# Performance work log

Hardware: AMD Instinct MI355X
Metric: run time of the kernel (lower is better)

Reference implementation:

```python
import jax, jax.numpy as jnp
import numpy as np

B, P, D, H, U, C = 32, 196, 512, 8, 4, 500

def setup_inputs() -> dict:
    key = jax.random.key(0)
    ks = jax.random.split(key, 12)
    s = 0.02
    return {
        "patch_embeddings": jax.random.normal(ks[0], (B, P, D), jnp.float32),
        "global_features": jax.random.normal(ks[1], (B, D), jnp.float32),
        "query_vectors": jax.random.normal(ks[2], (H, D), jnp.float32) * s,
        "dom_W": jax.random.normal(ks[3], (D, D), jnp.float32) / np.sqrt(D),
        "dom_b": jnp.zeros((D,), jnp.float32),
        "sem_W": jax.random.normal(ks[4], (H, D, D), jnp.float32) / np.sqrt(D),
        "sem_b": jnp.zeros((H, D), jnp.float32),
        "unknown_semantic_tokens": jax.random.normal(ks[5], (U, D), jnp.float32) * s,
        "known_prefix": jax.random.normal(ks[6], (C, 1, D), jnp.float32) * s,   # SOS embedding per class
        "known_suffix": jax.random.normal(ks[7], (C, 1, D), jnp.float32) * s,   # last-token embedding per class
        "unk_prefix": jax.random.normal(ks[8], (1, D), jnp.float32) * s,
        "unk_suffix": jax.random.normal(ks[9], (1, D), jnp.float32) * s,
    }


def reference(patch_embeddings, global_features, query_vectors, dom_W, dom_b,
              sem_W, sem_b, unknown_semantic_tokens, known_prefix, known_suffix,
              unk_prefix, unk_suffix):
    b, p, d = patch_embeddings.shape
    h = query_vectors.shape[0]
    c = known_prefix.shape[0]
    u = unknown_semantic_tokens.shape[0]

    # SemanticTokenExtractor: per-head attention over patches (vectorized over heads)
    scores = jnp.einsum('bpd,hd->bph', patch_embeddings, query_vectors)      # [B,P,H]
    weights = jax.nn.softmax(scores, axis=1)                                  # softmax over patches
    semantic_tokens = jnp.einsum('bph,bpd->bhd', weights, patch_embeddings)   # [B,H,D]

    # DomainTokenGenerator (2D input -> identity) + domain projection (torch Linear: x @ W.T + b)
    projected_domain = global_features @ dom_W.T + dom_b                      # [B,D]

    # Per-head semantic projections: head k uses its own Linear
    projected_sem = jnp.einsum('bhd,hed->bhe', semantic_tokens, sem_W) + sem_b  # [B,H,D]

    # Known prompts: for each (b, c): [prefix_c(1), domain_b(1), semantics_b(H), suffix_c(1)]
    pre = jnp.broadcast_to(known_prefix[None], (b, c, 1, d))
    dom = jnp.broadcast_to(projected_domain[:, None, None, :], (b, c, 1, d))
    sem = jnp.broadcast_to(projected_sem[:, None], (b, c, h, d))
    suf = jnp.broadcast_to(known_suffix[None], (b, c, 1, d))
    known_prompts = jnp.concatenate([pre, dom, sem, suf], axis=2).reshape(b * c, h + 3, d)

    # Unknown prompts: [unk_prefix(1), domain_b(1), unknown_semantic_tokens(U), unk_suffix(1)]
    upre = jnp.broadcast_to(unk_prefix[None], (b, 1, d))
    udom = projected_domain[:, None, :]
    usem = jnp.broadcast_to(unknown_semantic_tokens[None], (b, u, d))
    usuf = jnp.broadcast_to(unk_suffix[None], (b, 1, d))
    unknown_prompts = jnp.concatenate([upre, udom, usem, usuf], axis=1)       # [B, U+3, D]

    return known_prompts, unknown_prompts, semantic_tokens
```

## Files before the change

kernel.cpp:

```cpp
#include <hip/hip_runtime.h>

typedef unsigned int uint32;
typedef uint32 v4u __attribute__((ext_vector_type(4)));

#define Bb 32
#define Pp 196
#define Dd 512
#define Hh 8
#define Uu 4
#define Cc 500

#define OUT1_ELEM_OFF 90112000
#define OUT2_ELEM_OFF 90226688

#define NPC 16

#define WS_SC   0
#define WS_PART 51200
#define WS_DOM  2148352
#define WS_SEM  2164736

__device__ __forceinline__ float dot4(float4 a, float4 b, float acc) {
    acc = fmaf(a.x, b.x, acc);
    acc = fmaf(a.y, b.y, acc);
    acc = fmaf(a.z, b.z, acc);
    acc = fmaf(a.w, b.w, acc);
    return acc;
}

__global__ __launch_bounds__(256)
void k_scores(const float* __restrict__ patch, const float* __restrict__ query,
              float* __restrict__ sc) {
    __shared__ float s_q[Hh * Dd];
    const int b = blockIdx.x / 49;
    const int p0 = (blockIdx.x % 49) * 4;
    const int tid = threadIdx.x;
    for (int j = tid; j < Hh * Dd / 4; j += 256)
        ((float4*)s_q)[j] = ((const float4*)query)[j];
    __syncthreads();

    const int wave = tid >> 6, lane = tid & 63;
    const int p = p0 + wave;
    const float* pr = patch + ((size_t)b * Pp + p) * Dd + lane * 8;
    const float4 v0 = *(const float4*)pr;
    const float4 v1 = *(const float4*)(pr + 4);

    float out = 0.f;
#pragma unroll
    for (int h = 0; h < 8; ++h) {
        const float4 q0 = *(const float4*)&s_q[h * Dd + lane * 8];
        const float4 q1 = *(const float4*)&s_q[h * Dd + lane * 8 + 4];
        float a = dot4(v0, q0, 0.f);
        a = dot4(v1, q1, a);
#pragma unroll
        for (int m = 32; m >= 1; m >>= 1) a += __shfl_xor(a, m, 64);
        if (lane == h) out = a;
    }
    if (lane < 8) sc[((size_t)b * Hh + lane) * Pp + p] = out;
}

__global__ __launch_bounds__(256)
void k_pool_part(const float* __restrict__ patch, const float* __restrict__ sc,
                 float* __restrict__ part) {
    __shared__ float s_w[Hh * Pp];
    const int b = blockIdx.x >> 4;
    const int pc = blockIdx.x & 15;
    const int tid = threadIdx.x;

    for (int j = tid; j < Hh * Pp; j += 256) s_w[j] = sc[(size_t)b * Hh * Pp + j];
    __syncthreads();

    {
        const int h = tid >> 5, gl = tid & 31;
        float m = -1e30f;
        for (int p = gl; p < Pp; p += 32) m = fmaxf(m, s_w[h * Pp + p]);
#pragma unroll
        for (int mm = 16; mm >= 1; mm >>= 1) m = fmaxf(m, __shfl_xor(m, mm, 64));
        float s = 0.f;
        for (int p = gl; p < Pp; p += 32) s += __expf(s_w[h * Pp + p] - m);
#pragma unroll
        for (int mm = 16; mm >= 1; mm >>= 1) s += __shfl_xor(s, mm, 64);
        const float inv = 1.f / s;
        for (int p = gl; p < Pp; p += 32)
            s_w[h * Pp + p] = __expf(s_w[h * Pp + p] - m) * inv;
    }
    __syncthreads();

    const int f = tid & 127;
    const int hq = tid >> 7;
    const int pstart = pc * 13;
    const int pend = (pstart + 13 < Pp) ? pstart + 13 : Pp;
    float4 a0 = {0, 0, 0, 0}, a1 = a0, a2 = a0, a3 = a0;
    const float4* pb4 = (const float4*)(patch + (size_t)b * Pp * Dd);
    for (int p = pstart; p < pend; ++p) {
        const float4 pv = pb4[p * 128 + f];
        const float w0 = s_w[(hq * 4 + 0) * Pp + p];
        const float w1 = s_w[(hq * 4 + 1) * Pp + p];
        const float w2 = s_w[(hq * 4 + 2) * Pp + p];
        const float w3 = s_w[(hq * 4 + 3) * Pp + p];
        a0.x = fmaf(w0, pv.x, a0.x); a0.y = fmaf(w0, pv.y, a0.y);
        a0.z = fmaf(w0, pv.z, a0.z); a0.w = fmaf(w0, pv.w, a0.w);
        a1.x = fmaf(w1, pv.x, a1.x); a1.y = fmaf(w1, pv.y, a1.y);
        a1.z = fmaf(w1, pv.z, a1.z); a1.w = fmaf(w1, pv.w, a1.w);
        a2.x = fmaf(w2, pv.x, a2.x); a2.y = fmaf(w2, pv.y, a2.y);
        a2.z = fmaf(w2, pv.z, a2.z); a2.w = fmaf(w2, pv.w, a2.w);
        a3.x = fmaf(w3, pv.x, a3.x); a3.y = fmaf(w3, pv.y, a3.y);
        a3.z = fmaf(w3, pv.z, a3.z); a3.w = fmaf(w3, pv.w, a3.w);
    }
    float4* po = (float4*)part + ((size_t)b * NPC + pc) * 1024;
    po[(hq * 4 + 0) * 128 + f] = a0;
    po[(hq * 4 + 1) * 128 + f] = a1;
    po[(hq * 4 + 2) * 128 + f] = a2;
    po[(hq * 4 + 3) * 128 + f] = a3;
}

__global__ __launch_bounds__(256)
void k_combine(const float* __restrict__ part, float* __restrict__ st) {
    const int idx = blockIdx.x * 256 + threadIdx.x;
    const int b = idx >> 10;
    const int r = idx & 1023;
    const float4* p4 = (const float4*)part;
    float4 a = {0, 0, 0, 0};
#pragma unroll
    for (int pc = 0; pc < NPC; ++pc) {
        const float4 v = p4[((size_t)b * NPC + pc) * 1024 + r];
        a.x += v.x; a.y += v.y; a.z += v.z; a.w += v.w;
    }
    ((float4*)st)[idx] = a;
}

#define PJS 513
__global__ __launch_bounds__(256)
void k_proj(const float* __restrict__ gf, const float* __restrict__ domW,
            const float* __restrict__ domb, const float* __restrict__ semW,
            const float* __restrict__ semb, const float* __restrict__ st,
            float* __restrict__ dom_ws, float* __restrict__ sem_ws) {
    __shared__ float s_w[32 * PJS];
    __shared__ float s_st[32 * PJS];
    const int blk = blockIdx.x;
    const int tid = threadIdx.x;
    if (blk < 128) {
        const int h = blk >> 4;
        const int e0 = (blk & 15) * 32;
        for (int g = tid; g < 32 * 128; g += 256) {
            const int r = g >> 7, c4 = g & 127;
            const float4 w = ((const float4*)semW)[((size_t)(h * Dd + e0 + r)) * 128 + c4];
            float* dw = &s_w[r * PJS + c4 * 4];
            dw[0] = w.x; dw[1] = w.y; dw[2] = w.z; dw[3] = w.w;
            const float4 s = ((const float4*)st)[((size_t)(r * Hh + h)) * 128 + c4];
            float* ds = &s_st[r * PJS + c4 * 4];
            ds[0] = s.x; ds[1] = s.y; ds[2] = s.z; ds[3] = s.w;
        }
        __syncthreads();
        const int pe = tid & 15;
        const int pb = tid >> 4;
        const float* w0r = &s_w[(2 * pe) * PJS];
        const float* w1r = &s_w[(2 * pe + 1) * PJS];
        const float* s0r = &s_st[(2 * pb) * PJS];
        const float* s1r = &s_st[(2 * pb + 1) * PJS];
        float a00 = 0.f, a01 = 0.f, a10 = 0.f, a11 = 0.f;
#pragma unroll 8
        for (int d = 0; d < Dd; ++d) {
            const float w0 = w0r[d], w1 = w1r[d];
            const float s0 = s0r[d], s1 = s1r[d];
            a00 = fmaf(s0, w0, a00);
            a01 = fmaf(s0, w1, a01);
            a10 = fmaf(s1, w0, a10);
            a11 = fmaf(s1, w1, a11);
        }
        const int e_ = e0 + 2 * pe;
        const float b0 = semb[h * Dd + e_], b1 = semb[h * Dd + e_ + 1];
        float* o0 = &sem_ws[((2 * pb) * Hh + h) * Dd + e_];
        float* o1 = &sem_ws[((2 * pb + 1) * Hh + h) * Dd + e_];
        o0[0] = a00 + b0; o0[1] = a01 + b1;
        o1[0] = a10 + b0; o1[1] = a11 + b1;
    } else {
        const int tg = (blk - 128) * 256 + tid;
        const int b = tg >> 9;
        const int e = tg & 511;
        const float4* wr = (const float4*)(domW + (size_t)e * Dd);
        const float4* gr = (const float4*)(gf + (size_t)b * Dd);
        float acc = domb[e];
#pragma unroll 8
        for (int j = 0; j < Dd / 4; ++j) acc = dot4(gr[j], wr[j], acc);
        dom_ws[b * Dd + e] = acc;
    }
}

__global__ __launch_bounds__(256)
void k_assemble(const v4u* __restrict__ pre, const v4u* __restrict__ suf,
                const v4u* __restrict__ dom, const v4u* __restrict__ sem,
                const v4u* __restrict__ upre, const v4u* __restrict__ usuf,
                const v4u* __restrict__ ust,
                v4u* __restrict__ out0, v4u* __restrict__ out1) {
    const int blk = blockIdx.x;
    const int tid = threadIdx.x;
    if (blk < 16000) {
        const int b = blk / 500;
        const int c = blk % 500;
        v4u* row = out0 + (size_t)blk * 1408;
#pragma unroll
        for (int k = 0; k < 6; ++k) {
            const int i = tid + k * 256;
            if (k < 5 || i < 1408) {
                const int t = i >> 7;
                const int off = i & 127;
                v4u v;
                if (t == 0) v = pre[c * 128 + off];
                else if (t == 10) v = suf[c * 128 + off];
                else if (t == 1) v = dom[b * 128 + off];
                else v = sem[b * 1024 + (t - 2) * 128 + off];
                row[i] = v;
            }
        }
    } else {
        const int b = blk - 16000;
#pragma unroll
        for (int k = 0; k < 4; ++k) {
            const int i = tid + k * 256;
            if (k < 3 || i < 896) {
                const int t = i >> 7;
                const int off = i & 127;
                v4u v;
                if (t == 0) v = upre[off];
                else if (t == 6) v = usuf[off];
                else if (t == 1) v = dom[b * 128 + off];
                else v = ust[(t - 2) * 128 + off];
                out1[b * 896 + i] = v;
            }
        }
    }
}

extern "C" void kernel_launch(void* const* d_in, const int* in_sizes, int n_in,
                              void* d_out, int out_size, void* d_ws, size_t ws_size,
                              hipStream_t stream) {
    const float* patch = (const float*)d_in[0];
    const float* gf    = (const float*)d_in[1];
    const float* query = (const float*)d_in[2];
    const float* domW  = (const float*)d_in[3];
    const float* domb  = (const float*)d_in[4];
    const float* semW  = (const float*)d_in[5];
    const float* semb  = (const float*)d_in[6];
    const float* ust   = (const float*)d_in[7];
    const float* pre   = (const float*)d_in[8];
    const float* suf   = (const float*)d_in[9];
    const float* upre  = (const float*)d_in[10];
    const float* usuf  = (const float*)d_in[11];

    float* out = (float*)d_out;
    float* st_out = out + OUT2_ELEM_OFF;

    float* ws   = (float*)d_ws;
    float* sc_w = ws + WS_SC;
    float* part = ws + WS_PART;
    float* domp = ws + WS_DOM;
    float* semp = ws + WS_SEM;

    hipLaunchKernelGGL(k_scores, dim3(Bb * 49), dim3(256), 0, stream, patch, query, sc_w);
    hipLaunchKernelGGL(k_pool_part, dim3(Bb * NPC), dim3(256), 0, stream, patch, sc_w, part);
    hipLaunchKernelGGL(k_combine, dim3(128), dim3(256), 0, stream, part, st_out);
    hipLaunchKernelGGL(k_proj, dim3(192), dim3(256), 0, stream,
                       gf, domW, domb, semW, semb, st_out, domp, semp);
    hipLaunchKernelGGL(k_assemble, dim3(16032), dim3(256), 0, stream,
                       (const v4u*)pre, (const v4u*)suf,
                       (const v4u*)domp, (const v4u*)semp,
                       (const v4u*)upre, (const v4u*)usuf, (const v4u*)ust,
                       (v4u*)out, (v4u*)(out + OUT1_ELEM_OFF));
}
```

Baseline: 434.6 us.

## Restructure pooling, split-K semantic projection, and reorder assemble block mapping

Pooling blocks now use 128 threads, each accumulating all 8 heads, so every patch row is read once per block instead of twice. The semantic projection splits the reduction dimension in two across more blocks, using float4 shared tiles and a 4x2 register tile, and adds a small kernel that sums the partials and applies the bias. The assemble kernel moves to 128-thread blocks with one token row per iteration, and interleaves classes across consecutive blocks so the same batch's domain and semantic rows are reused. The cost is an extra kernel launch and a partial-sum buffer in workspace. Assemble, a write-bound copy of about 360 MB, dominates the run time.

```diff
diff --git a/kernel.cpp b/kernel.cpp
--- a/kernel.cpp
+++ b/kernel.cpp
@@ -19,6 +19,7 @@
 #define WS_PART 51200
 #define WS_DOM  2148352
 #define WS_SEM  2164736
+#define WS_PP   2295808
 
 __device__ __forceinline__ float dot4(float4 a, float4 b, float acc) {
     acc = fmaf(a.x, b.x, acc);
@@ -59,7 +60,7 @@
     if (lane < 8) sc[((size_t)b * Hh + lane) * Pp + p] = out;
 }
 
-__global__ __launch_bounds__(256)
+__global__ __launch_bounds__(128)
 void k_pool_part(const float* __restrict__ patch, const float* __restrict__ sc,
                  float* __restrict__ part) {
     __shared__ float s_w[Hh * Pp];
@@ -67,51 +68,46 @@
     const int pc = blockIdx.x & 15;
     const int tid = threadIdx.x;
 
-    for (int j = tid; j < Hh * Pp; j += 256) s_w[j] = sc[(size_t)b * Hh * Pp + j];
+    for (int j = tid; j < Hh * Pp; j += 128) s_w[j] = sc[(size_t)b * Hh * Pp + j];
     __syncthreads();
 
     {
-        const int h = tid >> 5, gl = tid & 31;
+        const int h = tid >> 4, gl = tid & 15;
         float m = -1e30f;
-        for (int p = gl; p < Pp; p += 32) m = fmaxf(m, s_w[h * Pp + p]);
-#pragma unroll
-        for (int mm = 16; mm >= 1; mm >>= 1) m = fmaxf(m, __shfl_xor(m, mm, 64));
+        for (int p = gl; p < Pp; p += 16) m = fmaxf(m, s_w[h * Pp + p]);
+#pragma unroll
+        for (int mm = 8; mm >= 1; mm >>= 1) m = fmaxf(m, __shfl_xor(m, mm, 64));
         float s = 0.f;
-        for (int p = gl; p < Pp; p += 32) s += __expf(s_w[h * Pp + p] - m);
-#pragma unroll
-        for (int mm = 16; mm >= 1; mm >>= 1) s += __shfl_xor(s, mm, 64);
+        for (int p = gl; p < Pp; p += 16) s += __expf(s_w[h * Pp + p] - m);
+#pragma unroll
+        for (int mm = 8; mm >= 1; mm >>= 1) s += __shfl_xor(s, mm, 64);
         const float inv = 1.f / s;
-        for (int p = gl; p < Pp; p += 32)
+        for (int p = gl; p < Pp; p += 16)
             s_w[h * Pp + p] = __expf(s_w[h * Pp + p] - m) * inv;
     }
     __syncthreads();
 
-    const int f = tid & 127;
-    const int hq = tid >> 7;
+    const int f = tid;
     const int pstart = pc * 13;
     const int pend = (pstart + 13 < Pp) ? pstart + 13 : Pp;
-    float4 a0 = {0, 0, 0, 0}, a1 = a0, a2 = a0, a3 = a0;
+    float4 acc[8];
+#pragma unroll
+    for (int h = 0; h < 8; ++h) acc[h] = (float4){0, 0, 0, 0};
     const float4* pb4 = (const float4*)(patch + (size_t)b * Pp * Dd);
     for (int p = pstart; p < pend; ++p) {
         const float4 pv = pb4[p * 128 + f];
-        const float w0 = s_w[(hq * 4 + 0) * Pp + p];
-        const float w1 = s_w[(hq * 4 + 1) * Pp + p];
-        const float w2 = s_w[(hq * 4 + 2) * Pp + p];
-        const float w3 = s_w[(hq * 4 + 3) * Pp + p];
-        a0.x = fmaf(w0, pv.x, a0.x); a0.y = fmaf(w0, pv.y, a0.y);
-        a0.z = fmaf(w0, pv.z, a0.z); a0.w = fmaf(w0, pv.w, a0.w);
-        a1.x = fmaf(w1, pv.x, a1.x); a1.y = fmaf(w1, pv.y, a1.y);
-        a1.z = fmaf(w1, pv.z, a1.z); a1.w = fmaf(w1, pv.w, a1.w);
-        a2.x = fmaf(w2, pv.x, a2.x); a2.y = fmaf(w2, pv.y, a2.y);
-        a2.z = fmaf(w2, pv.z, a2.z); a2.w = fmaf(w2, pv.w, a2.w);
-        a3.x = fmaf(w3, pv.x, a3.x); a3.y = fmaf(w3, pv.y, a3.y);
-        a3.z = fmaf(w3, pv.z, a3.z); a3.w = fmaf(w3, pv.w, a3.w);
+#pragma unroll
+        for (int h = 0; h < 8; ++h) {
+            const float w = s_w[h * Pp + p];
+            acc[h].x = fmaf(w, pv.x, acc[h].x);
+            acc[h].y = fmaf(w, pv.y, acc[h].y);
+            acc[h].z = fmaf(w, pv.z, acc[h].z);
+            acc[h].w = fmaf(w, pv.w, acc[h].w);
+        }
     }
     float4* po = (float4*)part + ((size_t)b * NPC + pc) * 1024;
-    po[(hq * 4 + 0) * 128 + f] = a0;
-    po[(hq * 4 + 1) * 128 + f] = a1;
-    po[(hq * 4 + 2) * 128 + f] = a2;
-    po[(hq * 4 + 3) * 128 + f] = a3;
+#pragma unroll
+    for (int h = 0; h < 8; ++h) po[h * 128 + f] = acc[h];
 }
 
 __global__ __launch_bounds__(256)
@@ -129,53 +125,53 @@
     ((float4*)st)[idx] = a;
 }
 
-#define PJS 513
-__global__ __launch_bounds__(256)
+__global__ __launch_bounds__(128)
 void k_proj(const float* __restrict__ gf, const float* __restrict__ domW,
             const float* __restrict__ domb, const float* __restrict__ semW,
-            const float* __restrict__ semb, const float* __restrict__ st,
-            float* __restrict__ dom_ws, float* __restrict__ sem_ws) {
-    __shared__ float s_w[32 * PJS];
-    __shared__ float s_st[32 * PJS];
+            const float* __restrict__ st,
+            float* __restrict__ dom_ws, float* __restrict__ pp) {
+    __shared__ float4 s_w4[32][65];
+    __shared__ float4 s_st4[32][65];
     const int blk = blockIdx.x;
     const int tid = threadIdx.x;
-    if (blk < 128) {
-        const int h = blk >> 4;
-        const int e0 = (blk & 15) * 32;
-        for (int g = tid; g < 32 * 128; g += 256) {
-            const int r = g >> 7, c4 = g & 127;
-            const float4 w = ((const float4*)semW)[((size_t)(h * Dd + e0 + r)) * 128 + c4];
-            float* dw = &s_w[r * PJS + c4 * 4];
-            dw[0] = w.x; dw[1] = w.y; dw[2] = w.z; dw[3] = w.w;
-            const float4 s = ((const float4*)st)[((size_t)(r * Hh + h)) * 128 + c4];
-            float* ds = &s_st[r * PJS + c4 * 4];
-            ds[0] = s.x; ds[1] = s.y; ds[2] = s.z; ds[3] = s.w;
+    if (blk < 256) {
+        const int h = blk >> 5;
+        const int et = (blk & 31) >> 1;
+        const int k = blk & 1;
+        const int e0 = et * 32;
+        for (int g = tid; g < 32 * 64; g += 128) {
+            const int r = g >> 6, c4 = g & 63;
+            s_w4[r][c4] = ((const float4*)semW)[(size_t)(h * Dd + e0 + r) * 128 + k * 64 + c4];
+            s_st4[r][c4] = ((const float4*)st)[(size_t)(r * Hh + h) * 128 + k * 64 + c4];
         }
         __syncthreads();
-        const int pe = tid & 15;
-        const int pb = tid >> 4;
-        const float* w0r = &s_w[(2 * pe) * PJS];
-        const float* w1r = &s_w[(2 * pe + 1) * PJS];
-        const float* s0r = &s_st[(2 * pb) * PJS];
-        const float* s1r = &s_st[(2 * pb + 1) * PJS];
-        float a00 = 0.f, a01 = 0.f, a10 = 0.f, a11 = 0.f;
-#pragma unroll 8
-        for (int d = 0; d < Dd; ++d) {
-            const float w0 = w0r[d], w1 = w1r[d];
-            const float s0 = s0r[d], s1 = s1r[d];
-            a00 = fmaf(s0, w0, a00);
-            a01 = fmaf(s0, w1, a01);
-            a10 = fmaf(s1, w0, a10);
-            a11 = fmaf(s1, w1, a11);
-        }
-        const int e_ = e0 + 2 * pe;
-        const float b0 = semb[h * Dd + e_], b1 = semb[h * Dd + e_ + 1];
-        float* o0 = &sem_ws[((2 * pb) * Hh + h) * Dd + e_];
-        float* o1 = &sem_ws[((2 * pb + 1) * Hh + h) * Dd + e_];
-        o0[0] = a00 + b0; o0[1] = a01 + b1;
-        o1[0] = a10 + b0; o1[1] = a11 + b1;
+        const int pe = tid & 7;
+        const int pb = tid >> 3;
+        const float4* w0 = s_w4[pe * 4 + 0];
+        const float4* w1 = s_w4[pe * 4 + 1];
+        const float4* w2 = s_w4[pe * 4 + 2];
+        const float4* w3 = s_w4[pe * 4 + 3];
+        const float4* sA = s_st4[2 * pb];
+        const float4* sB = s_st4[2 * pb + 1];
+        float4 accA = {0, 0, 0, 0}, accB = {0, 0, 0, 0};
+#pragma unroll 4
+        for (int d4 = 0; d4 < 64; ++d4) {
+            const float4 a = sA[d4];
+            const float4 b = sB[d4];
+            const float4 v0 = w0[d4];
+            const float4 v1 = w1[d4];
+            const float4 v2 = w2[d4];
+            const float4 v3 = w3[d4];
+            accA.x = dot4(a, v0, accA.x); accA.y = dot4(a, v1, accA.y);
+            accA.z = dot4(a, v2, accA.z); accA.w = dot4(a, v3, accA.w);
+            accB.x = dot4(b, v0, accB.x); accB.y = dot4(b, v1, accB.y);
+            accB.z = dot4(b, v2, accB.z); accB.w = dot4(b, v3, accB.w);
+        }
+        float4* o = (float4*)pp + (size_t)k * 32768;
+        o[((2 * pb) * Hh + h) * 128 + et * 8 + pe] = accA;
+        o[((2 * pb + 1) * Hh + h) * 128 + et * 8 + pe] = accB;
     } else {
-        const int tg = (blk - 128) * 256 + tid;
+        const int tg = (blk - 256) * 128 + tid;
         const int b = tg >> 9;
         const int e = tg & 511;
         const float4* wr = (const float4*)(domW + (size_t)e * Dd);
@@ -188,6 +184,21 @@
 }
 
 __global__ __launch_bounds__(256)
+void k_proj_sum(const float* __restrict__ pp, const float* __restrict__ semb,
+                float* __restrict__ sem_ws) {
+    const int idx4 = blockIdx.x * 256 + threadIdx.x;
+    const float4 a = ((const float4*)pp)[idx4];
+    const float4 b = ((const float4*)pp)[32768 + idx4];
+    const float4 bias = ((const float4*)semb)[idx4 & 1023];
+    float4 o;
+    o.x = a.x + b.x + bias.x;
+    o.y = a.y + b.y + bias.y;
+    o.z = a.z + b.z + bias.z;
+    o.w = a.w + b.w + bias.w;
+    ((float4*)sem_ws)[idx4] = o;
+}
+
+__global__ __launch_bounds__(128)
 void k_assemble(const v4u* __restrict__ pre, const v4u* __restrict__ suf,
                 const v4u* __restrict__ dom, const v4u* __restrict__ sem,
                 const v4u* __restrict__ upre, const v4u* __restrict__ usuf,
@@ -195,39 +206,32 @@
                 v4u* __restrict__ out0, v4u* __restrict__ out1) {
     const int blk = blockIdx.x;
     const int tid = threadIdx.x;
-    if (blk < 16000) {
-        const int b = blk / 500;
-        const int c = blk % 500;
-        v4u* row = out0 + (size_t)blk * 1408;
-#pragma unroll
-        for (int k = 0; k < 6; ++k) {
-            const int i = tid + k * 256;
-            if (k < 5 || i < 1408) {
-                const int t = i >> 7;
-                const int off = i & 127;
-                v4u v;
-                if (t == 0) v = pre[c * 128 + off];
-                else if (t == 10) v = suf[c * 128 + off];
-                else if (t == 1) v = dom[b * 128 + off];
-                else v = sem[b * 1024 + (t - 2) * 128 + off];
-                row[i] = v;
-            }
+    if (blk < 16128) {
+        const int x = blk & 7;
+        const int m = blk >> 3;
+        const int b = m / 63;
+        const int c = x + 8 * (m % 63);
+        if (c >= Cc) return;
+        v4u* row = out0 + (size_t)(b * Cc + c) * 1408;
+#pragma unroll
+        for (int t = 0; t < 11; ++t) {
+            v4u v;
+            if (t == 0) v = pre[c * 128 + tid];
+            else if (t == 10) v = suf[c * 128 + tid];
+            else if (t == 1) v = dom[b * 128 + tid];
+            else v = sem[b * 1024 + (t - 2) * 128 + tid];
+            row[t * 128 + tid] = v;
         }
     } else {
-        const int b = blk - 16000;
-#pragma unroll
-        for (int k = 0; k < 4; ++k) {
-            const int i = tid + k * 256;
-            if (k < 3 || i < 896) {
-                const int t = i >> 7;
-                const int off = i & 127;
-                v4u v;
-                if (t == 0) v = upre[off];
-                else if (t == 6) v = usuf[off];
-                else if (t == 1) v = dom[b * 128 + off];
-                else v = ust[(t - 2) * 128 + off];
-                out1[b * 896 + i] = v;
-            }
+        const int b = blk - 16128;
+#pragma unroll
+        for (int t = 0; t < 7; ++t) {
+            v4u v;
+            if (t == 0) v = upre[tid];
+            else if (t == 6) v = usuf[tid];
+            else if (t == 1) v = dom[b * 128 + tid];
+            else v = ust[(t - 2) * 128 + tid];
+            out1[b * 896 + t * 128 + tid] = v;
         }
     }
 }
@@ -256,13 +260,15 @@
     float* part = ws + WS_PART;
     float* domp = ws + WS_DOM;
     float* semp = ws + WS_SEM;
+    float* pp   = ws + WS_PP;
 
     hipLaunchKernelGGL(k_scores, dim3(Bb * 49), dim3(256), 0, stream, patch, query, sc_w);
-    hipLaunchKernelGGL(k_pool_part, dim3(Bb * NPC), dim3(256), 0, stream, patch, sc_w, part);
+    hipLaunchKernelGGL(k_pool_part, dim3(Bb * NPC), dim3(128), 0, stream, patch, sc_w, part);
     hipLaunchKernelGGL(k_combine, dim3(128), dim3(256), 0, stream, part, st_out);
-    hipLaunchKernelGGL(k_proj, dim3(192), dim3(256), 0, stream,
-                       gf, domW, domb, semW, semb, st_out, domp, semp);
-    hipLaunchKernelGGL(k_assemble, dim3(16032), dim3(256), 0, stream,
+    hipLaunchKernelGGL(k_proj, dim3(384), dim3(128), 0, stream,
+                       gf, domW, domb, semW, st_out, domp, pp);
+    hipLaunchKernelGGL(k_proj_sum, dim3(128), dim3(256), 0, stream, pp, semb, semp);
+    hipLaunchKernelGGL(k_assemble, dim3(16160), dim3(128), 0, stream,
                        (const v4u*)pre, (const v4u*)suf,
                        (const v4u*)domp, (const v4u*)semp,
                        (const v4u*)upre, (const v4u*)usuf, (const v4u*)ust,
```

Result: no change. 439.3 us (+1.1%).
